# Optimization experiments

Hardware: AMD Instinct MI355X
Metric: run time of the kernel (lower is better)

Reference implementation:

```python
import jax, jax.numpy as jnp
import numpy as np

DIM = 1024
D_STATE = 16
D_CONV = 4
EXPAND = 2
D_INNER = EXPAND * DIM
BATCH = 4
SEQ = 2048


def setup_inputs() -> dict:
    key = jax.random.key(0)
    ks = jax.random.split(key, 9)
    n = lambda i, shape, scale=0.02: (jax.random.normal(ks[i], shape, jnp.float32) * scale)
    return {
        "x": jax.random.normal(ks[0], (BATCH, SEQ, DIM), jnp.float32),
        "in_proj_w": n(1, (D_INNER, DIM)),
        "conv_w": n(2, (D_INNER, D_CONV), 0.1),          # depthwise kernel (groups=d_inner)
        "x_proj_w": n(3, (2 * D_STATE + 1, D_INNER)),
        "dt_proj_w": n(4, (D_INNER, 1), 1.0),
        "dt_proj_b": n(5, (D_INNER,), 0.1),
        "A_log": jax.random.normal(ks[6], (D_INNER, D_STATE), jnp.float32),
        "D": jnp.ones((D_INNER,), jnp.float32),
        "out_proj_w": n(7, (DIM, D_INNER)),
        "norm_w": jnp.ones((DIM,), jnp.float32),
        "norm_b": jnp.zeros((DIM,), jnp.float32),
    }


def reference(x, in_proj_w, conv_w, x_proj_w, dt_proj_w, dt_proj_b,
              A_log, D, out_proj_w, norm_w, norm_b):
    Bsz, L, _ = x.shape
    shortcut = x

    # LayerNorm
    mu = jnp.mean(x, axis=-1, keepdims=True)
    var = jnp.var(x, axis=-1, keepdims=True)
    h = (x - mu) / jnp.sqrt(var + 1e-5) * norm_w + norm_b

    # in_proj: [B,L,dim] -> [B,L,d_inner]
    h = h @ in_proj_w.T

    # causal depthwise conv1d (padding d_conv-1, truncate to L)
    hp = jnp.pad(h, ((0, 0), (D_CONV - 1, 0), (0, 0)))
    h_conv = sum(hp[:, k:k + L, :] * conv_w[:, k] for k in range(D_CONV))
    h = jax.nn.silu(h_conv)

    # x_proj -> dt (1), B (d_state), C (d_state)
    proj = h @ x_proj_w.T
    dt_in = proj[..., :1]
    B_param = proj[..., 1:1 + D_STATE]      # [B,L,d_state]
    C_param = proj[..., 1 + D_STATE:]       # [B,L,d_state]
    dt = jax.nn.softplus(dt_in @ dt_proj_w.T + dt_proj_b)  # [B,L,d_inner]

    A = -jnp.exp(A_log)                     # [d_inner, d_state]

    def step(state, inp):
        dt_t, B_t, C_t, x_t = inp           # [B,d_inner],[B,ds],[B,ds],[B,d_inner]
        state = jnp.exp(A[None] * dt_t[:, :, None]) * state \
                + B_t[:, None, :] * x_t[:, :, None]          # [B,d_inner,d_state]
        y = jnp.einsum('bnd,bd->bn', state, C_t) + D * x_t   # [B,d_inner]
        return state, y

    init = jnp.zeros((Bsz, D_INNER, D_STATE), x.dtype)
    xs = (jnp.swapaxes(dt, 0, 1), jnp.swapaxes(B_param, 0, 1),
          jnp.swapaxes(C_param, 0, 1), jnp.swapaxes(h, 0, 1))
    state, ys = jax.lax.scan(step, init, xs)
    y = jnp.swapaxes(ys, 0, 1)              # [B,L,d_inner]

    out = jax.nn.silu(y) @ out_proj_w.T + shortcut
    return out, state
```

## Files before the change

### kernel.cpp

```cpp
#include <hip/hip_runtime.h>

typedef unsigned short u16;
typedef unsigned int u32;
typedef __attribute__((ext_vector_type(8))) short short8;
typedef __attribute__((ext_vector_type(4))) float f32x4;
typedef __attribute__((ext_vector_type(2))) float f32x2;
typedef __attribute__((ext_vector_type(8))) unsigned short ushort8_t;

#define SEQ 2048
#define DIM 1024
#define DINNER 2048
#define NPROJ 33
#define NPROJ_PAD 48
#define LC 32
#define NC 64

__device__ __forceinline__ u16 f2bf(float f) {
  union { float f; u32 u; } v; v.f = f;
  u32 r = (v.u + 0x7fffu + ((v.u >> 16) & 1u)) >> 16;
  return (u16)r;
}
__device__ __forceinline__ float bf2f(u16 s) {
  union { u32 u; float f; } v; v.u = ((u32)s) << 16;
  return v.f;
}
__device__ __forceinline__ float lo_bf(u32 w) {
  union { u32 u; float f; } v; v.u = w << 16; return v.f;
}
__device__ __forceinline__ float hi_bf(u32 w) {
  union { u32 u; float f; } v; v.u = w & 0xffff0000u; return v.f;
}
__device__ __forceinline__ float fexp2(float x) {
#if __has_builtin(__builtin_amdgcn_exp2f)
  return __builtin_amdgcn_exp2f(x);
#else
  return __expf(x * 0.69314718f);
#endif
}
__device__ __forceinline__ float softplus(float x) {
  return fmaxf(x, 0.f) + __logf(1.f + __expf(-fabsf(x)));
}
__device__ __forceinline__ f32x2 sp2(float v) { f32x2 r; r.x = v; r.y = v; return r; }
__device__ __forceinline__ f32x2 pkfma(f32x2 a, f32x2 b, f32x2 c) {
  return __builtin_elementwise_fma(a, b, c);
}
__device__ __forceinline__ void async16(const void* g, void* l) {
  __builtin_amdgcn_global_load_lds(
      (const __attribute__((address_space(1))) u32*)g,
      (__attribute__((address_space(3))) u32*)l, 16, 0, 0);
}

__global__ void cast_w_kernel(const float* __restrict__ w1, const float* __restrict__ w3,
                              u16* __restrict__ o1, u16* __restrict__ o3) {
  int i = blockIdx.x * 256 + threadIdx.x;
  float4 a = ((const float4*)w1)[i];
  float4 b = ((const float4*)w3)[i];
  ushort4 oa, ob;
  oa.x = f2bf(a.x); oa.y = f2bf(a.y); oa.z = f2bf(a.z); oa.w = f2bf(a.w);
  ob.x = f2bf(b.x); ob.y = f2bf(b.y); ob.z = f2bf(b.z); ob.w = f2bf(b.w);
  ((ushort4*)o1)[i] = oa;
  ((ushort4*)o3)[i] = ob;
}

__global__ void cast_w2pad_kernel(const float* __restrict__ src, u16* __restrict__ dst) {
  int i = blockIdx.x * 256 + threadIdx.x;
  int j = i >> 11, k = i & 2047;
  dst[i] = (j < NPROJ) ? f2bf(src[j * 2048 + k]) : (u16)0;
}

__global__ __launch_bounds__(256) void ln_kernel(const float* __restrict__ x,
                                                 const float* __restrict__ w,
                                                 const float* __restrict__ b,
                                                 u16* __restrict__ h) {
  const int row = blockIdx.x;
  const int tid = threadIdx.x;
  const int lane = tid & 63, wave = tid >> 6;
  const float4 v = ((const float4*)(x + (size_t)row * DIM))[tid];
  float s = v.x + v.y + v.z + v.w;
  float q = v.x * v.x + v.y * v.y + v.z * v.z + v.w * v.w;
  for (int off = 32; off; off >>= 1) {
    s += __shfl_down(s, off);
    q += __shfl_down(q, off);
  }
  __shared__ float sbuf[8];
  if (lane == 0) { sbuf[wave] = s; sbuf[4 + wave] = q; }
  __syncthreads();
  float tot = sbuf[0] + sbuf[1] + sbuf[2] + sbuf[3];
  float totq = sbuf[4] + sbuf[5] + sbuf[6] + sbuf[7];
  const float mean = tot * (1.0f / DIM);
  const float var = totq * (1.0f / DIM) - mean * mean;
  const float rs = rsqrtf(var + 1e-5f);
  const float4 wv = ((const float4*)w)[tid];
  const float4 bv = ((const float4*)b)[tid];
  ushort4 o;
  o.x = f2bf((v.x - mean) * rs * wv.x + bv.x);
  o.y = f2bf((v.y - mean) * rs * wv.y + bv.y);
  o.z = f2bf((v.z - mean) * rs * wv.z + bv.z);
  o.w = f2bf((v.w - mean) * rs * wv.w + bv.w);
  ((ushort4*)(h + (size_t)row * DIM))[tid] = o;
}

__global__ __launch_bounds__(512) void gemm_bf16_kernel(const u16* __restrict__ A,
                                                        const u16* __restrict__ Bt,
                                                        u16* __restrict__ C,
                                                        int K, int N) {
  __shared__ u16 As[128 * 32];
  __shared__ u16 Bs[128 * 32];
  const int tid = threadIdx.x;
  const int lane = tid & 63, wave = tid >> 6;
  const int wm = wave >> 2, wn = wave & 3;
  const int row16 = lane & 15, quad = lane >> 4;
  const int flat = blockIdx.x + gridDim.x * blockIdx.y;
  const int xcd = flat & 7;
  const int sidx = flat >> 3;
  const int bm = xcd * 8 + (sidx & 7);
  const int bn = sidx >> 3;
  f32x4 acc[4][2] = {};
  const u16* Ablk = A + (size_t)bm * 128 * K;
  const u16* Bblk = Bt + (size_t)bn * 128 * K;
  const int r = tid >> 2, cc = (tid & 3) * 8;
  for (int k0 = 0; k0 < K; k0 += 32) {
    async16(Ablk + (size_t)r * K + k0 + cc, &As[tid * 8]);
    async16(Bblk + (size_t)r * K + k0 + cc, &Bs[tid * 8]);
    __syncthreads();
    short8 af[4], bfr[2];
#pragma unroll
    for (int i = 0; i < 4; ++i)
      af[i] = *(const short8*)&As[(wm * 64 + i * 16 + row16) * 32 + quad * 8];
#pragma unroll
    for (int j = 0; j < 2; ++j)
      bfr[j] = *(const short8*)&Bs[(wn * 32 + j * 16 + row16) * 32 + quad * 8];
#pragma unroll
    for (int i = 0; i < 4; ++i)
#pragma unroll
      for (int j = 0; j < 2; ++j)
        acc[i][j] = __builtin_amdgcn_mfma_f32_16x16x32_bf16(af[i], bfr[j], acc[i][j], 0, 0, 0);
    __syncthreads();
  }
#pragma unroll
  for (int i = 0; i < 4; ++i) {
    int m = bm * 128 + wm * 64 + i * 16 + quad * 4;
#pragma unroll
    for (int j = 0; j < 2; ++j) {
      int n = bn * 128 + wn * 32 + j * 16 + row16;
#pragma unroll
      for (int rr = 0; rr < 4; ++rr)
        C[(size_t)(m + rr) * N + n] = f2bf(acc[i][j][rr]);
    }
  }
}

__global__ __launch_bounds__(512) void gemm_out_kernel(const u16* __restrict__ A,
                                                       const u16* __restrict__ Bt,
                                                       const float* __restrict__ resid,
                                                       float* __restrict__ C,
                                                       int K, int N) {
  __shared__ u16 As[128 * 32];
  __shared__ u16 Bs[128 * 32];
  const int tid = threadIdx.x;
  const int lane = tid & 63, wave = tid >> 6;
  const int wm = wave >> 2, wn = wave & 3;
  const int row16 = lane & 15, quad = lane >> 4;
  const int flat = blockIdx.x + gridDim.x * blockIdx.y;
  const int xcd = flat & 7;
  const int sidx = flat >> 3;
  const int bm = xcd * 8 + (sidx & 7);
  const int bn = sidx >> 3;
  f32x4 acc[4][2] = {};
  const u16* Ablk = A + (size_t)bm * 128 * K;
  const u16* Bblk = Bt + (size_t)bn * 128 * K;
  const int r = tid >> 2, cc = (tid & 3) * 8;
  for (int k0 = 0; k0 < K; k0 += 32) {
    async16(Ablk + (size_t)r * K + k0 + cc, &As[tid * 8]);
    async16(Bblk + (size_t)r * K + k0 + cc, &Bs[tid * 8]);
    __syncthreads();
    short8 af[4], bfr[2];
#pragma unroll
    for (int i = 0; i < 4; ++i)
      af[i] = *(const short8*)&As[(wm * 64 + i * 16 + row16) * 32 + quad * 8];
#pragma unroll
    for (int j = 0; j < 2; ++j)
      bfr[j] = *(const short8*)&Bs[(wn * 32 + j * 16 + row16) * 32 + quad * 8];
#pragma unroll
    for (int i = 0; i < 4; ++i)
#pragma unroll
      for (int j = 0; j < 2; ++j)
        acc[i][j] = __builtin_amdgcn_mfma_f32_16x16x32_bf16(af[i], bfr[j], acc[i][j], 0, 0, 0);
    __syncthreads();
  }
#pragma unroll
  for (int i = 0; i < 4; ++i) {
    int m = bm * 128 + wm * 64 + i * 16 + quad * 4;
#pragma unroll
    for (int j = 0; j < 2; ++j) {
      int n = bn * 128 + wn * 32 + j * 16 + row16;
#pragma unroll
      for (int rr = 0; rr < 4; ++rr) {
        size_t idx = (size_t)(m + rr) * N + n;
        C[idx] = acc[i][j][rr] + resid[idx];
      }
    }
  }
}

__global__ __launch_bounds__(256) void conv_silu_kernel(const u16* __restrict__ c1,
                                                        const float* __restrict__ cw,
                                                        u16* __restrict__ cs) {
  const int tid = threadIdx.x;
  const int dg = tid * 8;
  const size_t m0 = (size_t)blockIdx.x * 8;
  const int l0 = (int)(m0 & (SEQ - 1));
  float w[4][8];
  {
    const float4* cw4 = (const float4*)(cw + (size_t)dg * 4);
#pragma unroll
    for (int c = 0; c < 8; ++c) {
      float4 v = cw4[c];
      w[0][c] = v.x; w[1][c] = v.y; w[2][c] = v.z; w[3][c] = v.w;
    }
  }
  const u16* base = c1 + m0 * DINNER + dg;
  ushort8_t win0, win1, win2, win3;
  const ushort8_t zero = (ushort8_t)0;
  if (l0 == 0) {
    win0 = zero; win1 = zero; win2 = zero;
  } else {
    win0 = *(const ushort8_t*)(base - 3 * DINNER);
    win1 = *(const ushort8_t*)(base - 2 * DINNER);
    win2 = *(const ushort8_t*)(base - 1 * DINNER);
  }
  win3 = *(const ushort8_t*)(base);
#pragma unroll
  for (int t = 0; t < 8; ++t) {
    ushort8_t nxt = win3;
    if (t < 7) nxt = *(const ushort8_t*)(base + (size_t)(t + 1) * DINNER);
    ushort8_t o;
#pragma unroll
    for (int c = 0; c < 8; ++c) {
      float acc = bf2f((u16)win0[c]) * w[0][c];
      acc = fmaf(bf2f((u16)win1[c]), w[1][c], acc);
      acc = fmaf(bf2f((u16)win2[c]), w[2][c], acc);
      acc = fmaf(bf2f((u16)win3[c]), w[3][c], acc);
      const float s = acc / (1.f + __expf(-acc));
      o[c] = (unsigned short)f2bf(s);
    }
    *(ushort8_t*)(cs + (m0 + t) * DINNER + dg) = o;
    win0 = win1; win1 = win2; win2 = win3; win3 = nxt;
  }
}

__global__ __launch_bounds__(256) void gemm_w2_kernel(const u16* __restrict__ A,
                                                      const u16* __restrict__ Bt,
                                                      float* __restrict__ C) {
  __shared__ u16 As[64 * 32];
  __shared__ u16 Bs[48 * 32];
  const int tid = threadIdx.x;
  const int lane = tid & 63, wave = tid >> 6;
  const int row16 = lane & 15, quad = lane >> 4;
  const int bm = blockIdx.x;
  const int K = DINNER;
  f32x4 acc[3] = {};
  const u16* Ablk = A + (size_t)bm * 64 * K;
  const int r = tid >> 2, cc = (tid & 3) * 8;
  for (int k0 = 0; k0 < K; k0 += 32) {
    async16(Ablk + (size_t)r * K + k0 + cc, &As[tid * 8]);
    if (tid < 192) async16(Bt + (size_t)r * K + k0 + cc, &Bs[tid * 8]);
    __syncthreads();
    short8 af = *(const short8*)&As[(wave * 16 + row16) * 32 + quad * 8];
    short8 bfr[3];
#pragma unroll
    for (int j = 0; j < 3; ++j)
      bfr[j] = *(const short8*)&Bs[(j * 16 + row16) * 32 + quad * 8];
#pragma unroll
    for (int j = 0; j < 3; ++j)
      acc[j] = __builtin_amdgcn_mfma_f32_16x16x32_bf16(af, bfr[j], acc[j], 0, 0, 0);
    __syncthreads();
  }
  const int m = bm * 64 + wave * 16 + quad * 4;
#pragma unroll
  for (int j = 0; j < 3; ++j) {
    const int n = j * 16 + row16;
#pragma unroll
    for (int rr = 0; rr < 4; ++rr)
      C[(size_t)(m + rr) * NPROJ_PAD + n] = acc[j][rr];
  }
}


__global__ __launch_bounds__(128) void scan_phase1(const float* __restrict__ proj,
                                                   const u16* __restrict__ xs,
                                                   const float* __restrict__ dtw_,
                                                   const float* __restrict__ dtb_,
                                                   const float* __restrict__ A_log,
                                                   u16* __restrict__ S,
                                                   float* __restrict__ Tdt) {
  __shared__ float Bsh[LC][16];
  __shared__ float DTin[LC];
  const int tid = threadIdx.x;
  const int d0 = blockIdx.x * 256 + tid * 2;
  const int c = blockIdx.y;
  const int b = blockIdx.z;
  const size_t mrow = (size_t)b * SEQ + c * LC;
  for (int i = tid; i < LC * 16; i += 128) {
    int t = i >> 4, n = i & 15;
    Bsh[t][n] = proj[(mrow + t) * NPROJ_PAD + 1 + n];
  }
  if (tid < LC) DTin[tid] = proj[(mrow + tid) * NPROJ_PAD];
  __syncthreads();
  f32x2 An2[16];
#pragma unroll
  for (int n = 0; n < 16; ++n) {
    An2[n].x = -__expf(A_log[(size_t)d0 * 16 + n]) * 1.44269504f;
    An2[n].y = -__expf(A_log[(size_t)(d0 + 1) * 16 + n]) * 1.44269504f;
  }
  const float2 dtwv = *(const float2*)(dtw_ + d0);
  const float2 dtbv = *(const float2*)(dtb_ + d0);
  f32x2 dtw2; dtw2.x = dtwv.x; dtw2.y = dtwv.y;
  f32x2 dtb2; dtb2.x = dtbv.x; dtb2.y = dtbv.y;
  f32x2 s[16];
#pragma unroll
  for (int n = 0; n < 16; ++n) s[n] = sp2(0.f);
  f32x2 Tsum = sp2(0.f);
  const u16* xp = xs + mrow * DINNER + d0;
  u32 xw = *(const u32*)xp;
#pragma unroll 2
  for (int t = 0; t < LC; ++t) {
    f32x2 xv; xv.x = lo_bf(xw); xv.y = hi_bf(xw);
    if (t + 1 < LC) xw = *(const u32*)(xp + (size_t)(t + 1) * DINNER);
    f32x2 dtv = pkfma(sp2(DTin[t]), dtw2, dtb2);
    f32x2 sp; sp.x = softplus(dtv.x); sp.y = softplus(dtv.y);
    Tsum += sp;
    const float4* Br = (const float4*)&Bsh[t][0];
#pragma unroll
    for (int q = 0; q < 4; ++q) {
      const float4 Bq = Br[q];
      const float bqa[4] = {Bq.x, Bq.y, Bq.z, Bq.w};
#pragma unroll
      for (int j = 0; j < 4; ++j) {
        const int n = q * 4 + j;
        f32x2 e = An2[n] * sp;
        f32x2 dk; dk.x = fexp2(e.x); dk.y = fexp2(e.y);
        s[n] = pkfma(dk, s[n], sp2(bqa[j]) * xv);
      }
    }
  }
  const size_t so = ((size_t)(b * NC + c) * DINNER + d0) * 16;
  ushort8_t o0, o1, o2, o3;
#pragma unroll
  for (int j = 0; j < 8; ++j) {
    o0[j] = f2bf(s[j].x);     o1[j] = f2bf(s[8 + j].x);
    o2[j] = f2bf(s[j].y);     o3[j] = f2bf(s[8 + j].y);
  }
  *(ushort8_t*)(S + so) = o0;       *(ushort8_t*)(S + so + 8) = o1;
  *(ushort8_t*)(S + so + 16) = o2;  *(ushort8_t*)(S + so + 24) = o3;
  *(float2*)(Tdt + (size_t)(b * NC + c) * DINNER + d0) = make_float2(Tsum.x, Tsum.y);
}

__global__ __launch_bounds__(256) void scan_phase2(const float* __restrict__ A_log,
                                                   u16* __restrict__ S,
                                                   const float* __restrict__ Tdt,
                                                   float* __restrict__ out_state) {
  const int idx = blockIdx.x * 256 + threadIdx.x;
  const int nq = idx & 3;
  const int d = (idx >> 2) & (DINNER - 1);
  const int b = idx >> 13;
  float An2[4];
#pragma unroll
  for (int n = 0; n < 4; ++n) An2[n] = -__expf(A_log[d * 16 + nq * 4 + n]) * 1.44269504f;
  float prev[4] = {0.f, 0.f, 0.f, 0.f};
  for (int c = 0; c < NC; ++c) {
    const size_t base = (size_t)(b * NC + c) * DINNER + d;
    const float T = Tdt[base];
    const size_t so = base * 16 + nq * 4;
    ushort4 lv = *(const ushort4*)(S + so);
    const float loc[4] = {bf2f(lv.x), bf2f(lv.y), bf2f(lv.z), bf2f(lv.w)};
    ushort4 pv;
    pv.x = f2bf(prev[0]); pv.y = f2bf(prev[1]); pv.z = f2bf(prev[2]); pv.w = f2bf(prev[3]);
    *(ushort4*)(S + so) = pv;
    const float dk0 = fexp2(An2[0] * T), dk1 = fexp2(An2[1] * T);
    const float dk2 = fexp2(An2[2] * T), dk3 = fexp2(An2[3] * T);
    prev[0] = fmaf(dk0, prev[0], loc[0]);
    prev[1] = fmaf(dk1, prev[1], loc[1]);
    prev[2] = fmaf(dk2, prev[2], loc[2]);
    prev[3] = fmaf(dk3, prev[3], loc[3]);
  }
  *(float4*)(out_state + ((size_t)b * DINNER + d) * 16 + nq * 4) =
      make_float4(prev[0], prev[1], prev[2], prev[3]);
}

__global__ __launch_bounds__(128) void scan_phase3(const float* __restrict__ proj,
                                                   const u16* __restrict__ xs,
                                                   const float* __restrict__ dtw_,
                                                   const float* __restrict__ dtb_,
                                                   const float* __restrict__ A_log,
                                                   const float* __restrict__ Dp,
                                                   const u16* __restrict__ S,
                                                   u16* __restrict__ ysil) {
  __shared__ float Bsh[LC][16];
  __shared__ float Csh[LC][16];
  __shared__ float DTin[LC];
  const int tid = threadIdx.x;
  const int d0 = blockIdx.x * 256 + tid * 2;
  const int c = blockIdx.y;
  const int b = blockIdx.z;
  const size_t mrow = (size_t)b * SEQ + c * LC;
  for (int i = tid; i < LC * 16; i += 128) {
    int t = i >> 4, n = i & 15;
    Bsh[t][n] = proj[(mrow + t) * NPROJ_PAD + 1 + n];
    Csh[t][n] = proj[(mrow + t) * NPROJ_PAD + 17 + n];
  }
  if (tid < LC) DTin[tid] = proj[(mrow + tid) * NPROJ_PAD];
  __syncthreads();
  f32x2 An2[16];
#pragma unroll
  for (int n = 0; n < 16; ++n) {
    An2[n].x = -__expf(A_log[(size_t)d0 * 16 + n]) * 1.44269504f;
    An2[n].y = -__expf(A_log[(size_t)(d0 + 1) * 16 + n]) * 1.44269504f;
  }
  const float2 dtwv = *(const float2*)(dtw_ + d0);
  const float2 dtbv = *(const float2*)(dtb_ + d0);
  const float2 Ddv = *(const float2*)(Dp + d0);
  f32x2 dtw2; dtw2.x = dtwv.x; dtw2.y = dtwv.y;
  f32x2 dtb2; dtb2.x = dtbv.x; dtb2.y = dtbv.y;
  f32x2 Dd2; Dd2.x = Ddv.x; Dd2.y = Ddv.y;
  f32x2 s[16];
  const size_t so = ((size_t)(b * NC + c) * DINNER + d0) * 16;
  {
    ushort8_t v0 = *(const ushort8_t*)(S + so);
    ushort8_t v1 = *(const ushort8_t*)(S + so + 8);
    ushort8_t v2 = *(const ushort8_t*)(S + so + 16);
    ushort8_t v3 = *(const ushort8_t*)(S + so + 24);
#pragma unroll
    for (int j = 0; j < 8; ++j) {
      s[j].x = bf2f((u16)v0[j]);     s[8 + j].x = bf2f((u16)v1[j]);
      s[j].y = bf2f((u16)v2[j]);     s[8 + j].y = bf2f((u16)v3[j]);
    }
  }
  const u16* xp = xs + mrow * DINNER + d0;
  u16* yp = ysil + mrow * DINNER + d0;
  u32 xw = *(const u32*)xp;
#pragma unroll 2
  for (int t = 0; t < LC; ++t) {
    f32x2 xv; xv.x = lo_bf(xw); xv.y = hi_bf(xw);
    if (t + 1 < LC) xw = *(const u32*)(xp + (size_t)(t + 1) * DINNER);
    f32x2 dtv = pkfma(sp2(DTin[t]), dtw2, dtb2);
    f32x2 sp; sp.x = softplus(dtv.x); sp.y = softplus(dtv.y);
    f32x2 y = Dd2 * xv;
    const float4* Br = (const float4*)&Bsh[t][0];
    const float4* Cr = (const float4*)&Csh[t][0];
#pragma unroll
    for (int q = 0; q < 4; ++q) {
      const float4 Bq = Br[q];
      const float4 Cq = Cr[q];
      const float bqa[4] = {Bq.x, Bq.y, Bq.z, Bq.w};
      const float cqa[4] = {Cq.x, Cq.y, Cq.z, Cq.w};
#pragma unroll
      for (int j = 0; j < 4; ++j) {
        const int n = q * 4 + j;
        f32x2 e = An2[n] * sp;
        f32x2 dk; dk.x = fexp2(e.x); dk.y = fexp2(e.y);
        s[n] = pkfma(dk, s[n], sp2(bqa[j]) * xv);
        y = pkfma(sp2(cqa[j]), s[n], y);
      }
    }
    const float sy0 = y.x / (1.f + __expf(-y.x));
    const float sy1 = y.y / (1.f + __expf(-y.y));
    const u32 ow = (u32)f2bf(sy0) | ((u32)f2bf(sy1) << 16);
    *(u32*)(yp + (size_t)t * DINNER) = ow;
  }
}

extern "C" void kernel_launch(void* const* d_in, const int* in_sizes, int n_in,
                              void* d_out, int out_size, void* d_ws, size_t ws_size,
                              hipStream_t stream) {
  const float* x = (const float*)d_in[0];
  const float* in_proj_w = (const float*)d_in[1];
  const float* conv_w = (const float*)d_in[2];
  const float* x_proj_w = (const float*)d_in[3];
  const float* dt_proj_w = (const float*)d_in[4];
  const float* dt_proj_b = (const float*)d_in[5];
  const float* A_log = (const float*)d_in[6];
  const float* Dvec = (const float*)d_in[7];
  const float* out_proj_w = (const float*)d_in[8];
  const float* norm_w = (const float*)d_in[9];
  const float* norm_b = (const float*)d_in[10];

  char* ws = (char*)d_ws;
  u16* h = (u16*)(ws + 0);
  u16* w1b = (u16*)(ws + 16777216);
  u16* w3b = (u16*)(ws + 20971520);
  u16* w2b = (u16*)(ws + 25165824);
  u16* c1 = (u16*)(ws + 25362432);
  u16* ysil = c1;
  u16* cs = (u16*)(ws + 58916864);
  float* proj = (float*)(ws + 92471296);
  u16* Sbuf = (u16*)(ws + 94044160);
  float* Tdt = (float*)(ws + 110821376);

  float* out = (float*)d_out;
  float* out_state = out + (size_t)4 * SEQ * DIM;

  cast_w_kernel<<<2048, 256, 0, stream>>>(in_proj_w, out_proj_w, w1b, w3b);
  cast_w2pad_kernel<<<384, 256, 0, stream>>>(x_proj_w, w2b);
  ln_kernel<<<8192, 256, 0, stream>>>(x, norm_w, norm_b, h);
  gemm_bf16_kernel<<<dim3(DINNER / 128, 64), 512, 0, stream>>>(h, w1b, c1, DIM, DINNER);
  conv_silu_kernel<<<1024, 256, 0, stream>>>(c1, conv_w, cs);
  gemm_w2_kernel<<<128, 256, 0, stream>>>(cs, w2b, proj);
  scan_phase1<<<dim3(DINNER / 256, NC, 4), 128, 0, stream>>>(proj, cs, dt_proj_w, dt_proj_b,
                                                             A_log, Sbuf, Tdt);
  scan_phase2<<<128, 256, 0, stream>>>(A_log, Sbuf, Tdt, out_state);
  scan_phase3<<<dim3(DINNER / 256, NC, 4), 128, 0, stream>>>(proj, cs, dt_proj_w, dt_proj_b,
                                                             A_log, Dvec, Sbuf, ysil);
  gemm_out_kernel<<<dim3(DIM / 128, 64), 512, 0, stream>>>(ysil, w3b, x, out, DINNER, DIM);
}
```

Before: 379.0 us.

## Split scan state across thread pairs and widen small-kernel grids

The chunked scan phases 1 and 3 now split the 16 state channels across two adjacent threads, each holding 8. This doubles the threads per block and halves register pressure. In phase 3 the partial y sums are combined with a lane shuffle before the D skip term and SiLU are applied. Phase 2 now gives each thread one state element instead of four, gemm_w2 uses 32-row tiles with 128 threads to launch twice as many blocks, and SiLU divisions use a hardware reciprocal. Together these aim to raise occupancy and parallelism in latency-bound kernels, at the cost of duplicated softplus work, extra shuffles, and a slightly less accurate reciprocal.

```diff
diff --git a/kernel.cpp b/kernel.cpp
--- a/kernel.cpp
+++ b/kernel.cpp
@@ -35,6 +35,13 @@
   return __builtin_amdgcn_exp2f(x);
 #else
   return __expf(x * 0.69314718f);
+#endif
+}
+__device__ __forceinline__ float frcp(float x) {
+#if __has_builtin(__builtin_amdgcn_rcpf)
+  return __builtin_amdgcn_rcpf(x);
+#else
+  return 1.f / x;
 #endif
 }
 __device__ __forceinline__ float softplus(float x) {
@@ -241,7 +248,7 @@
       acc = fmaf(bf2f((u16)win1[c]), w[1][c], acc);
       acc = fmaf(bf2f((u16)win2[c]), w[2][c], acc);
       acc = fmaf(bf2f((u16)win3[c]), w[3][c], acc);
-      const float s = acc / (1.f + __expf(-acc));
+      const float s = acc * frcp(1.f + __expf(-acc));
       o[c] = (unsigned short)f2bf(s);
     }
     *(ushort8_t*)(cs + (m0 + t) * DINNER + dg) = o;
@@ -249,10 +256,10 @@
   }
 }
 
-__global__ __launch_bounds__(256) void gemm_w2_kernel(const u16* __restrict__ A,
+__global__ __launch_bounds__(128) void gemm_w2_kernel(const u16* __restrict__ A,
                                                       const u16* __restrict__ Bt,
                                                       float* __restrict__ C) {
-  __shared__ u16 As[64 * 32];
+  __shared__ u16 As[32 * 32];
   __shared__ u16 Bs[48 * 32];
   const int tid = threadIdx.x;
   const int lane = tid & 63, wave = tid >> 6;
@@ -260,11 +267,13 @@
   const int bm = blockIdx.x;
   const int K = DINNER;
   f32x4 acc[3] = {};
-  const u16* Ablk = A + (size_t)bm * 64 * K;
+  const u16* Ablk = A + (size_t)bm * 32 * K;
   const int r = tid >> 2, cc = (tid & 3) * 8;
   for (int k0 = 0; k0 < K; k0 += 32) {
     async16(Ablk + (size_t)r * K + k0 + cc, &As[tid * 8]);
-    if (tid < 192) async16(Bt + (size_t)r * K + k0 + cc, &Bs[tid * 8]);
+    async16(Bt + (size_t)r * K + k0 + cc, &Bs[tid * 8]);
+    if (tid < 64)
+      async16(Bt + (size_t)(32 + r) * K + k0 + cc, &Bs[1024 + tid * 8]);
     __syncthreads();
     short8 af = *(const short8*)&As[(wave * 16 + row16) * 32 + quad * 8];
     short8 bfr[3];
@@ -276,7 +285,7 @@
       acc[j] = __builtin_amdgcn_mfma_f32_16x16x32_bf16(af, bfr[j], acc[j], 0, 0, 0);
     __syncthreads();
   }
-  const int m = bm * 64 + wave * 16 + quad * 4;
+  const int m = bm * 32 + wave * 16 + quad * 4;
 #pragma unroll
   for (int j = 0; j < 3; ++j) {
     const int n = j * 16 + row16;
@@ -287,7 +296,7 @@
 }
 
 
-__global__ __launch_bounds__(128) void scan_phase1(const float* __restrict__ proj,
+__global__ __launch_bounds__(256) void scan_phase1(const float* __restrict__ proj,
                                                    const u16* __restrict__ xs,
                                                    const float* __restrict__ dtw_,
                                                    const float* __restrict__ dtb_,
@@ -297,29 +306,31 @@
   __shared__ float Bsh[LC][16];
   __shared__ float DTin[LC];
   const int tid = threadIdx.x;
-  const int d0 = blockIdx.x * 256 + tid * 2;
+  const int p = tid >> 1, nh = tid & 1;
+  const int nbase = nh * 8;
+  const int d0 = blockIdx.x * 256 + p * 2;
   const int c = blockIdx.y;
   const int b = blockIdx.z;
   const size_t mrow = (size_t)b * SEQ + c * LC;
-  for (int i = tid; i < LC * 16; i += 128) {
+  for (int i = tid; i < LC * 16; i += 256) {
     int t = i >> 4, n = i & 15;
     Bsh[t][n] = proj[(mrow + t) * NPROJ_PAD + 1 + n];
   }
   if (tid < LC) DTin[tid] = proj[(mrow + tid) * NPROJ_PAD];
   __syncthreads();
-  f32x2 An2[16];
-#pragma unroll
-  for (int n = 0; n < 16; ++n) {
-    An2[n].x = -__expf(A_log[(size_t)d0 * 16 + n]) * 1.44269504f;
-    An2[n].y = -__expf(A_log[(size_t)(d0 + 1) * 16 + n]) * 1.44269504f;
+  f32x2 An2[8];
+#pragma unroll
+  for (int j = 0; j < 8; ++j) {
+    An2[j].x = -__expf(A_log[(size_t)d0 * 16 + nbase + j]) * 1.44269504f;
+    An2[j].y = -__expf(A_log[(size_t)(d0 + 1) * 16 + nbase + j]) * 1.44269504f;
   }
   const float2 dtwv = *(const float2*)(dtw_ + d0);
   const float2 dtbv = *(const float2*)(dtb_ + d0);
   f32x2 dtw2; dtw2.x = dtwv.x; dtw2.y = dtwv.y;
   f32x2 dtb2; dtb2.x = dtbv.x; dtb2.y = dtbv.y;
-  f32x2 s[16];
-#pragma unroll
-  for (int n = 0; n < 16; ++n) s[n] = sp2(0.f);
+  f32x2 s[8];
+#pragma unroll
+  for (int j = 0; j < 8; ++j) s[j] = sp2(0.f);
   f32x2 Tsum = sp2(0.f);
   const u16* xp = xs + mrow * DINNER + d0;
   u32 xw = *(const u32*)xp;
@@ -330,10 +341,11 @@
     f32x2 dtv = pkfma(sp2(DTin[t]), dtw2, dtb2);
     f32x2 sp; sp.x = softplus(dtv.x); sp.y = softplus(dtv.y);
     Tsum += sp;
-    const float4* Br = (const float4*)&Bsh[t][0];
-#pragma unroll
-    for (int q = 0; q < 4; ++q) {
-      const float4 Bq = Br[q];
+    const float4* Br = (const float4*)&Bsh[t][nbase];
+    const float4 B0 = Br[0], B1 = Br[1];
+#pragma unroll
+    for (int q = 0; q < 2; ++q) {
+      const float4 Bq = q ? B1 : B0;
       const float bqa[4] = {Bq.x, Bq.y, Bq.z, Bq.w};
 #pragma unroll
       for (int j = 0; j < 4; ++j) {
@@ -344,16 +356,17 @@
       }
     }
   }
-  const size_t so = ((size_t)(b * NC + c) * DINNER + d0) * 16;
-  ushort8_t o0, o1, o2, o3;
+  const size_t so = ((size_t)(b * NC + c) * DINNER + d0) * 16 + nbase;
+  ushort8_t o0, o1;
 #pragma unroll
   for (int j = 0; j < 8; ++j) {
-    o0[j] = f2bf(s[j].x);     o1[j] = f2bf(s[8 + j].x);
-    o2[j] = f2bf(s[j].y);     o3[j] = f2bf(s[8 + j].y);
-  }
-  *(ushort8_t*)(S + so) = o0;       *(ushort8_t*)(S + so + 8) = o1;
-  *(ushort8_t*)(S + so + 16) = o2;  *(ushort8_t*)(S + so + 24) = o3;
-  *(float2*)(Tdt + (size_t)(b * NC + c) * DINNER + d0) = make_float2(Tsum.x, Tsum.y);
+    o0[j] = f2bf(s[j].x);
+    o1[j] = f2bf(s[j].y);
+  }
+  *(ushort8_t*)(S + so) = o0;
+  *(ushort8_t*)(S + so + 16) = o1;
+  if (nh == 0)
+    *(float2*)(Tdt + (size_t)(b * NC + c) * DINNER + d0) = make_float2(Tsum.x, Tsum.y);
 }
 
 __global__ __launch_bounds__(256) void scan_phase2(const float* __restrict__ A_log,
@@ -361,34 +374,24 @@
                                                    const float* __restrict__ Tdt,
                                                    float* __restrict__ out_state) {
   const int idx = blockIdx.x * 256 + threadIdx.x;
-  const int nq = idx & 3;
-  const int d = (idx >> 2) & (DINNER - 1);
-  const int b = idx >> 13;
-  float An2[4];
-#pragma unroll
-  for (int n = 0; n < 4; ++n) An2[n] = -__expf(A_log[d * 16 + nq * 4 + n]) * 1.44269504f;
-  float prev[4] = {0.f, 0.f, 0.f, 0.f};
+  const int n = idx & 15;
+  const int d = (idx >> 4) & (DINNER - 1);
+  const int b = idx >> 15;
+  const float An = -__expf(A_log[d * 16 + n]) * 1.44269504f;
+  float prev = 0.f;
+#pragma unroll 4
   for (int c = 0; c < NC; ++c) {
     const size_t base = (size_t)(b * NC + c) * DINNER + d;
     const float T = Tdt[base];
-    const size_t so = base * 16 + nq * 4;
-    ushort4 lv = *(const ushort4*)(S + so);
-    const float loc[4] = {bf2f(lv.x), bf2f(lv.y), bf2f(lv.z), bf2f(lv.w)};
-    ushort4 pv;
-    pv.x = f2bf(prev[0]); pv.y = f2bf(prev[1]); pv.z = f2bf(prev[2]); pv.w = f2bf(prev[3]);
-    *(ushort4*)(S + so) = pv;
-    const float dk0 = fexp2(An2[0] * T), dk1 = fexp2(An2[1] * T);
-    const float dk2 = fexp2(An2[2] * T), dk3 = fexp2(An2[3] * T);
-    prev[0] = fmaf(dk0, prev[0], loc[0]);
-    prev[1] = fmaf(dk1, prev[1], loc[1]);
-    prev[2] = fmaf(dk2, prev[2], loc[2]);
-    prev[3] = fmaf(dk3, prev[3], loc[3]);
-  }
-  *(float4*)(out_state + ((size_t)b * DINNER + d) * 16 + nq * 4) =
-      make_float4(prev[0], prev[1], prev[2], prev[3]);
-}
-
-__global__ __launch_bounds__(128) void scan_phase3(const float* __restrict__ proj,
+    const size_t so = base * 16 + n;
+    const float loc = bf2f(S[so]);
+    S[so] = f2bf(prev);
+    prev = fmaf(fexp2(An * T), prev, loc);
+  }
+  out_state[((size_t)b * DINNER + d) * 16 + n] = prev;
+}
+
+__global__ __launch_bounds__(256) void scan_phase3(const float* __restrict__ proj,
                                                    const u16* __restrict__ xs,
                                                    const float* __restrict__ dtw_,
                                                    const float* __restrict__ dtb_,
@@ -400,40 +403,39 @@
   __shared__ float Csh[LC][16];
   __shared__ float DTin[LC];
   const int tid = threadIdx.x;
-  const int d0 = blockIdx.x * 256 + tid * 2;
+  const int p = tid >> 1, nh = tid & 1;
+  const int nbase = nh * 8;
+  const int d0 = blockIdx.x * 256 + p * 2;
   const int c = blockIdx.y;
   const int b = blockIdx.z;
   const size_t mrow = (size_t)b * SEQ + c * LC;
-  for (int i = tid; i < LC * 16; i += 128) {
+  for (int i = tid; i < LC * 16; i += 256) {
     int t = i >> 4, n = i & 15;
     Bsh[t][n] = proj[(mrow + t) * NPROJ_PAD + 1 + n];
     Csh[t][n] = proj[(mrow + t) * NPROJ_PAD + 17 + n];
   }
   if (tid < LC) DTin[tid] = proj[(mrow + tid) * NPROJ_PAD];
   __syncthreads();
-  f32x2 An2[16];
-#pragma unroll
-  for (int n = 0; n < 16; ++n) {
-    An2[n].x = -__expf(A_log[(size_t)d0 * 16 + n]) * 1.44269504f;
-    An2[n].y = -__expf(A_log[(size_t)(d0 + 1) * 16 + n]) * 1.44269504f;
+  f32x2 An2[8];
+#pragma unroll
+  for (int j = 0; j < 8; ++j) {
+    An2[j].x = -__expf(A_log[(size_t)d0 * 16 + nbase + j]) * 1.44269504f;
+    An2[j].y = -__expf(A_log[(size_t)(d0 + 1) * 16 + nbase + j]) * 1.44269504f;
   }
   const float2 dtwv = *(const float2*)(dtw_ + d0);
   const float2 dtbv = *(const float2*)(dtb_ + d0);
   const float2 Ddv = *(const float2*)(Dp + d0);
   f32x2 dtw2; dtw2.x = dtwv.x; dtw2.y = dtwv.y;
   f32x2 dtb2; dtb2.x = dtbv.x; dtb2.y = dtbv.y;
-  f32x2 Dd2; Dd2.x = Ddv.x; Dd2.y = Ddv.y;
-  f32x2 s[16];
-  const size_t so = ((size_t)(b * NC + c) * DINNER + d0) * 16;
+  f32x2 s[8];
+  const size_t so = ((size_t)(b * NC + c) * DINNER + d0) * 16 + nbase;
   {
     ushort8_t v0 = *(const ushort8_t*)(S + so);
-    ushort8_t v1 = *(const ushort8_t*)(S + so + 8);
-    ushort8_t v2 = *(const ushort8_t*)(S + so + 16);
-    ushort8_t v3 = *(const ushort8_t*)(S + so + 24);
+    ushort8_t v1 = *(const ushort8_t*)(S + so + 16);
 #pragma unroll
     for (int j = 0; j < 8; ++j) {
-      s[j].x = bf2f((u16)v0[j]);     s[8 + j].x = bf2f((u16)v1[j]);
-      s[j].y = bf2f((u16)v2[j]);     s[8 + j].y = bf2f((u16)v3[j]);
+      s[j].x = bf2f((u16)v0[j]);
+      s[j].y = bf2f((u16)v1[j]);
     }
   }
   const u16* xp = xs + mrow * DINNER + d0;
@@ -445,13 +447,15 @@
     if (t + 1 < LC) xw = *(const u32*)(xp + (size_t)(t + 1) * DINNER);
     f32x2 dtv = pkfma(sp2(DTin[t]), dtw2, dtb2);
     f32x2 sp; sp.x = softplus(dtv.x); sp.y = softplus(dtv.y);
-    f32x2 y = Dd2 * xv;
-    const float4* Br = (const float4*)&Bsh[t][0];
-    const float4* Cr = (const float4*)&Csh[t][0];
-#pragma unroll
-    for (int q = 0; q < 4; ++q) {
-      const float4 Bq = Br[q];
-      const float4 Cq = Cr[q];
+    f32x2 y = sp2(0.f);
+    const float4* Br = (const float4*)&Bsh[t][nbase];
+    const float4* Cr = (const float4*)&Csh[t][nbase];
+    const float4 B0 = Br[0], B1 = Br[1];
+    const float4 C0 = Cr[0], C1 = Cr[1];
+#pragma unroll
+    for (int q = 0; q < 2; ++q) {
+      const float4 Bq = q ? B1 : B0;
+      const float4 Cq = q ? C1 : C0;
       const float bqa[4] = {Bq.x, Bq.y, Bq.z, Bq.w};
       const float cqa[4] = {Cq.x, Cq.y, Cq.z, Cq.w};
 #pragma unroll
@@ -463,10 +467,16 @@
         y = pkfma(sp2(cqa[j]), s[n], y);
       }
     }
-    const float sy0 = y.x / (1.f + __expf(-y.x));
-    const float sy1 = y.y / (1.f + __expf(-y.y));
-    const u32 ow = (u32)f2bf(sy0) | ((u32)f2bf(sy1) << 16);
-    *(u32*)(yp + (size_t)t * DINNER) = ow;
+    float ry0 = y.x + __shfl_xor(y.x, 1);
+    float ry1 = y.y + __shfl_xor(y.y, 1);
+    ry0 = fmaf(Ddv.x, xv.x, ry0);
+    ry1 = fmaf(Ddv.y, xv.y, ry1);
+    const float sy0 = ry0 * frcp(1.f + __expf(-ry0));
+    const float sy1 = ry1 * frcp(1.f + __expf(-ry1));
+    if (nh == 0) {
+      const u32 ow = (u32)f2bf(sy0) | ((u32)f2bf(sy1) << 16);
+      *(u32*)(yp + (size_t)t * DINNER) = ow;
+    }
   }
 }
 
@@ -505,11 +515,11 @@
   ln_kernel<<<8192, 256, 0, stream>>>(x, norm_w, norm_b, h);
   gemm_bf16_kernel<<<dim3(DINNER / 128, 64), 512, 0, stream>>>(h, w1b, c1, DIM, DINNER);
   conv_silu_kernel<<<1024, 256, 0, stream>>>(c1, conv_w, cs);
-  gemm_w2_kernel<<<128, 256, 0, stream>>>(cs, w2b, proj);
-  scan_phase1<<<dim3(DINNER / 256, NC, 4), 128, 0, stream>>>(proj, cs, dt_proj_w, dt_proj_b,
+  gemm_w2_kernel<<<256, 128, 0, stream>>>(cs, w2b, proj);
+  scan_phase1<<<dim3(DINNER / 256, NC, 4), 256, 0, stream>>>(proj, cs, dt_proj_w, dt_proj_b,
                                                              A_log, Sbuf, Tdt);
-  scan_phase2<<<128, 256, 0, stream>>>(A_log, Sbuf, Tdt, out_state);
-  scan_phase3<<<dim3(DINNER / 256, NC, 4), 128, 0, stream>>>(proj, cs, dt_proj_w, dt_proj_b,
+  scan_phase2<<<512, 256, 0, stream>>>(A_log, Sbuf, Tdt, out_state);
+  scan_phase3<<<dim3(DINNER / 256, NC, 4), 256, 0, stream>>>(proj, cs, dt_proj_w, dt_proj_b,
                                                              A_log, Dvec, Sbuf, ysil);
   gemm_out_kernel<<<dim3(DIM / 128, 64), 512, 0, stream>>>(ysil, w3b, x, out, DINNER, DIM);
 }
```

After: 386.3 us. Within noise of the previous version (+2.0%).
